# Kernel optimization log

Measured on AMD Instinct MI355X. Metric: run time of the kernel, lower is better.

The kernel has to match this reference:

```python
import jax, jax.numpy as jnp
import numpy as np

N_NODES = 100000
N_EDGES = 3200000
IN_FEATS, HID_FEATS, OUT_FEATS = 256, 128, 64


def setup_inputs() -> dict:
    key = jax.random.key(0)
    k1, k2, k3, k4, k5 = jax.random.split(key, 5)
    x = jax.random.normal(k1, (N_NODES, IN_FEATS), dtype=jnp.float32)
    edge_src = jax.random.randint(k2, (N_EDGES,), 0, N_NODES, dtype=jnp.int64)
    edge_dst = jax.random.randint(k3, (N_EDGES,), 0, N_NODES, dtype=jnp.int64)
    # weights initialized like nn.Parameter(th.randn(...))
    W1 = jax.random.normal(k4, (IN_FEATS, HID_FEATS), dtype=jnp.float32)
    W2 = jax.random.normal(k5, (HID_FEATS, OUT_FEATS), dtype=jnp.float32)
    return {"x": x, "edge_src": edge_src, "edge_dst": edge_dst, "W1": W1, "W2": W2}


def _spmm_sum(h, edge_src, edge_dst, n_nodes):
    # gspmmv with norm flags False: out[d] = sum_{(s,d) in E} h[s]
    msgs = h[edge_src]  # [E, F] gather
    return jax.ops.segment_sum(msgs, edge_dst, num_segments=n_nodes)


def reference(x, edge_src, edge_dst, W1, W2):
    n = x.shape[0]
    h = x @ W1                                  # [N, hid]
    h = _spmm_sum(h, edge_src, edge_dst, n)     # SpMM aggregation
    h = jax.nn.relu(h)
    h = h @ W2                                  # [N, out]
    h = _spmm_sum(h, edge_src, edge_dst, n)
    return h
```

## Files before the change

kernel.cpp:

```cpp
#include <hip/hip_runtime.h>
#include <hip/hip_bf16.h>

#define N_NODES   100000
#define IN_F      256
#define HID_F     128
#define OUT_F     64

#define SCAN_CHUNK 512
#define NSCAN_BLK ((N_NODES + SCAN_CHUNK - 1) / SCAN_CHUNK)

#define NGROUP    8
#define GRANGE    (N_NODES / NGROUP)
#define FILL_BLKS 2048

__device__ __forceinline__ ushort f2bf(float f) {
    uint u = __float_as_uint(f);
    u += 0x7fffu + ((u >> 16) & 1u);
    return (ushort)(u >> 16);
}
__device__ __forceinline__ float bf2f_lo(uint u) { return __uint_as_float(u << 16); }
__device__ __forceinline__ float bf2f_hi(uint u) { return __uint_as_float(u & 0xffff0000u); }

__global__ __launch_bounds__(256) void gemm1_kernel(const float* __restrict__ x,
                                                    const float* __restrict__ W1,
                                                    ushort* __restrict__ h1) {
    __shared__ float xs[32][IN_F];
    const int tid = threadIdx.x;
    const int block_row = blockIdx.x * 32;

    {
        const float4* xg = reinterpret_cast<const float4*>(x + (size_t)block_row * IN_F);
        float4* xsv = reinterpret_cast<float4*>(&xs[0][0]);
#pragma unroll
        for (int i = 0; i < 8; ++i) {
            int idx = tid + i * 256;
            xsv[idx] = xg[idx];
        }
    }
    __syncthreads();

    const int cg = tid & 31;
    const int rg = tid >> 5;

    float acc[4][4] = {};
#pragma unroll 4
    for (int k = 0; k < IN_F; ++k) {
        const float4 w = *reinterpret_cast<const float4*>(W1 + (size_t)k * HID_F + cg * 4);
#pragma unroll
        for (int r = 0; r < 4; ++r) {
            const float xv = xs[rg * 4 + r][k];
            acc[r][0] = fmaf(xv, w.x, acc[r][0]);
            acc[r][1] = fmaf(xv, w.y, acc[r][1]);
            acc[r][2] = fmaf(xv, w.z, acc[r][2]);
            acc[r][3] = fmaf(xv, w.w, acc[r][3]);
        }
    }

#pragma unroll
    for (int r = 0; r < 4; ++r) {
        uint2 o;
        o.x = ((uint)f2bf(acc[r][1]) << 16) | (uint)f2bf(acc[r][0]);
        o.y = ((uint)f2bf(acc[r][3]) << 16) | (uint)f2bf(acc[r][2]);
        *reinterpret_cast<uint2*>(h1 + (size_t)(block_row + rg * 4 + r) * HID_F + cg * 4) = o;
    }
}

__global__ __launch_bounds__(256) void gemm2_kernel(const ushort* __restrict__ agg1,
                                                    const float* __restrict__ W2,
                                                    ushort* __restrict__ h2) {
    __shared__ float as_[32][HID_F];
    const int tid = threadIdx.x;
    const int block_row = blockIdx.x * 32;

    {
        const uint* ag = reinterpret_cast<const uint*>(agg1 + (size_t)block_row * HID_F);
        float* asf = &as_[0][0];
#pragma unroll
        for (int i = 0; i < 8; ++i) {
            int idx = tid + i * 256;
            uint u = ag[idx];
            asf[2 * idx]     = fmaxf(bf2f_lo(u), 0.f);
            asf[2 * idx + 1] = fmaxf(bf2f_hi(u), 0.f);
        }
    }
    __syncthreads();

    const int cg = tid & 15;
    const int rg = tid >> 4;

    float acc[2][4] = {};
#pragma unroll 4
    for (int k = 0; k < HID_F; ++k) {
        const float4 w = *reinterpret_cast<const float4*>(W2 + (size_t)k * OUT_F + cg * 4);
#pragma unroll
        for (int r = 0; r < 2; ++r) {
            const float xv = as_[rg * 2 + r][k];
            acc[r][0] = fmaf(xv, w.x, acc[r][0]);
            acc[r][1] = fmaf(xv, w.y, acc[r][1]);
            acc[r][2] = fmaf(xv, w.z, acc[r][2]);
            acc[r][3] = fmaf(xv, w.w, acc[r][3]);
        }
    }

#pragma unroll
    for (int r = 0; r < 2; ++r) {
        uint2 o;
        o.x = ((uint)f2bf(acc[r][1]) << 16) | (uint)f2bf(acc[r][0]);
        o.y = ((uint)f2bf(acc[r][3]) << 16) | (uint)f2bf(acc[r][2]);
        *reinterpret_cast<uint2*>(h2 + (size_t)(block_row + rg * 2 + r) * OUT_F + cg * 4) = o;
    }
}

__global__ __launch_bounds__(256) void hist_kernel(const int* __restrict__ dst,
                                                   int* __restrict__ counts, int n_edges) {
    int i = blockIdx.x * blockDim.x + threadIdx.x;
    const int stride = gridDim.x * blockDim.x;
    for (; i < n_edges; i += stride) atomicAdd(&counts[dst[i]], 1);
}

__global__ __launch_bounds__(256) void scan_reduce(const int* __restrict__ counts,
                                                   int* __restrict__ partials, int n) {
    __shared__ int sm[256];
    const int base = blockIdx.x * SCAN_CHUNK;
    const int t = threadIdx.x;
    int v = 0;
    for (int i = t; i < SCAN_CHUNK; i += 256) {
        int idx = base + i;
        if (idx < n) v += counts[idx];
    }
    sm[t] = v;
    __syncthreads();
    for (int off = 128; off > 0; off >>= 1) {
        if (t < off) sm[t] += sm[t + off];
        __syncthreads();
    }
    if (t == 0) partials[blockIdx.x] = sm[0];
}

__global__ __launch_bounds__(256) void scan_partials(const int* __restrict__ partials,
                                                     int* __restrict__ blockoff, int n) {
    __shared__ int a[256], b[256];
    const int t = threadIdx.x;
    a[t] = (t < n) ? partials[t] : 0;
    __syncthreads();
    int* cur = a; int* nxt = b;
    for (int off = 1; off < 256; off <<= 1) {
        nxt[t] = cur[t] + (t >= off ? cur[t - off] : 0);
        __syncthreads();
        int* tmp = cur; cur = nxt; nxt = tmp;
    }
    if (t < n) blockoff[t] = (t > 0) ? cur[t - 1] : 0;
}

__global__ __launch_bounds__(256) void scan_final(const int* __restrict__ counts,
                                                  const int* __restrict__ blockoff,
                                                  int* __restrict__ row_ptr,
                                                  int* __restrict__ cursor,
                                                  int n, int n_edges) {
    __shared__ int a[SCAN_CHUNK], b[SCAN_CHUNK];
    const int base = blockIdx.x * SCAN_CHUNK;
    const int t = threadIdx.x;
    for (int i = t; i < SCAN_CHUNK; i += 256) {
        int idx = base + i;
        a[i] = (idx < n) ? counts[idx] : 0;
    }
    __syncthreads();
    int* cur = a; int* nxt = b;
    for (int off = 1; off < SCAN_CHUNK; off <<= 1) {
        for (int i = t; i < SCAN_CHUNK; i += 256)
            nxt[i] = cur[i] + (i >= off ? cur[i - off] : 0);
        __syncthreads();
        int* tmp = cur; cur = nxt; nxt = tmp;
    }
    const int boff = blockoff[blockIdx.x];
    for (int i = t; i < SCAN_CHUNK; i += 256) {
        int idx = base + i;
        if (idx < n) {
            int ex = boff + (i > 0 ? cur[i - 1] : 0);
            row_ptr[idx] = ex;
            cursor[idx]  = ex;
        }
    }
    if (blockIdx.x == 0 && t == 0) row_ptr[n] = n_edges;
}

__global__ __launch_bounds__(256) void fill_part_kernel(const int* __restrict__ src,
                                                        const int* __restrict__ dst,
                                                        int* __restrict__ cursor,
                                                        int* __restrict__ csr_src,
                                                        int n_edges) {
    const int g  = blockIdx.x & (NGROUP - 1);
    const int lb = blockIdx.x >> 3;
    const int lo = g * GRANGE;
    const int hi = lo + GRANGE;
    const int stride = (FILL_BLKS / NGROUP) * 256;
    for (int i = lb * 256 + threadIdx.x; i < n_edges; i += stride) {
        const int d = __builtin_nontemporal_load(dst + i);
        if (d >= lo && d < hi) {
            const int s = __builtin_nontemporal_load(src + i);
            const int pos = atomicAdd(&cursor[d], 1);
            csr_src[pos] = s;
        }
    }
}

__global__ __launch_bounds__(256) void spmm1_kernel(const ushort* __restrict__ h,
                                                    const int* __restrict__ row_ptr,
                                                    const int* __restrict__ csr_src,
                                                    ushort* __restrict__ outb,
                                                    int n_nodes) {
    const int wid = blockIdx.x * 4 + (threadIdx.x >> 6);
    const int lane = threadIdx.x & 63;
    if (wid >= n_nodes) return;
    const int half = lane >> 5;
    const int sub  = lane & 31;

    const int beg = __builtin_amdgcn_readfirstlane(row_ptr[wid]);
    const int end = __builtin_amdgcn_readfirstlane(row_ptr[wid + 1]);

    float a0 = 0.f, a1 = 0.f, a2 = 0.f, a3 = 0.f;
    int j = beg;
#pragma unroll 2
    for (; j + 3 < end; j += 4) {
        const int s0 = __builtin_amdgcn_readfirstlane(csr_src[j + 0]);
        const int s1 = __builtin_amdgcn_readfirstlane(csr_src[j + 1]);
        const int s2 = __builtin_amdgcn_readfirstlane(csr_src[j + 2]);
        const int s3 = __builtin_amdgcn_readfirstlane(csr_src[j + 3]);
        const int sa = half ? s1 : s0;
        const int sb = half ? s3 : s2;
        const uint2 u = *reinterpret_cast<const uint2*>(h + (size_t)sa * HID_F + sub * 4);
        const uint2 v = *reinterpret_cast<const uint2*>(h + (size_t)sb * HID_F + sub * 4);
        a0 += bf2f_lo(u.x) + bf2f_lo(v.x);
        a1 += bf2f_hi(u.x) + bf2f_hi(v.x);
        a2 += bf2f_lo(u.y) + bf2f_lo(v.y);
        a3 += bf2f_hi(u.y) + bf2f_hi(v.y);
    }
    if (j + 1 < end) {
        const int s0 = __builtin_amdgcn_readfirstlane(csr_src[j + 0]);
        const int s1 = __builtin_amdgcn_readfirstlane(csr_src[j + 1]);
        const int sa = half ? s1 : s0;
        const uint2 u = *reinterpret_cast<const uint2*>(h + (size_t)sa * HID_F + sub * 4);
        a0 += bf2f_lo(u.x); a1 += bf2f_hi(u.x);
        a2 += bf2f_lo(u.y); a3 += bf2f_hi(u.y);
        j += 2;
    }
    if (j < end && half == 0) {
        const int s = csr_src[j];
        const uint2 u = *reinterpret_cast<const uint2*>(h + (size_t)s * HID_F + sub * 4);
        a0 += bf2f_lo(u.x); a1 += bf2f_hi(u.x);
        a2 += bf2f_lo(u.y); a3 += bf2f_hi(u.y);
    }

    a0 += __shfl_xor(a0, 32);
    a1 += __shfl_xor(a1, 32);
    a2 += __shfl_xor(a2, 32);
    a3 += __shfl_xor(a3, 32);

    if (half == 0) {
        uint2 o;
        o.x = ((uint)f2bf(a1) << 16) | (uint)f2bf(a0);
        o.y = ((uint)f2bf(a3) << 16) | (uint)f2bf(a2);
        *reinterpret_cast<uint2*>(outb + (size_t)wid * HID_F + sub * 4) = o;
    }
}

__global__ __launch_bounds__(256) void spmm2_kernel(const ushort* __restrict__ h,
                                                    const int* __restrict__ row_ptr,
                                                    const int* __restrict__ csr_src,
                                                    float* __restrict__ out,
                                                    int n_nodes) {
    const int wid = blockIdx.x * 4 + (threadIdx.x >> 6);
    const int lane = threadIdx.x & 63;
    if (wid >= n_nodes) return;
    const int q   = lane >> 4;
    const int sub = lane & 15;

    const int beg = __builtin_amdgcn_readfirstlane(row_ptr[wid]);
    const int end = __builtin_amdgcn_readfirstlane(row_ptr[wid + 1]);

    float a0 = 0.f, a1 = 0.f, a2 = 0.f, a3 = 0.f;
    int j = beg;
#pragma unroll 2
    for (; j + 3 < end; j += 4) {
        const int s0 = __builtin_amdgcn_readfirstlane(csr_src[j + 0]);
        const int s1 = __builtin_amdgcn_readfirstlane(csr_src[j + 1]);
        const int s2 = __builtin_amdgcn_readfirstlane(csr_src[j + 2]);
        const int s3 = __builtin_amdgcn_readfirstlane(csr_src[j + 3]);
        const int sel01 = (q & 1) ? s1 : s0;
        const int sel23 = (q & 1) ? s3 : s2;
        const int sa    = (q & 2) ? sel23 : sel01;
        const uint2 u = *reinterpret_cast<const uint2*>(h + (size_t)sa * OUT_F + sub * 4);
        a0 += bf2f_lo(u.x); a1 += bf2f_hi(u.x);
        a2 += bf2f_lo(u.y); a3 += bf2f_hi(u.y);
    }
    {
        const int rem = end - j;
        if (q < rem) {
            const int s = csr_src[j + q];
            const uint2 u = *reinterpret_cast<const uint2*>(h + (size_t)s * OUT_F + sub * 4);
            a0 += bf2f_lo(u.x); a1 += bf2f_hi(u.x);
            a2 += bf2f_lo(u.y); a3 += bf2f_hi(u.y);
        }
    }

    a0 += __shfl_xor(a0, 16); a1 += __shfl_xor(a1, 16);
    a2 += __shfl_xor(a2, 16); a3 += __shfl_xor(a3, 16);
    a0 += __shfl_xor(a0, 32); a1 += __shfl_xor(a1, 32);
    a2 += __shfl_xor(a2, 32); a3 += __shfl_xor(a3, 32);

    if (q == 0) {
        float4 o = make_float4(a0, a1, a2, a3);
        *reinterpret_cast<float4*>(out + (size_t)wid * OUT_F + sub * 4) = o;
    }
}

extern "C" void kernel_launch(void* const* d_in, const int* in_sizes, int n_in,
                              void* d_out, int out_size, void* d_ws, size_t ws_size,
                              hipStream_t stream) {
    const float* x    = (const float*)d_in[0];
    const int*   esrc = (const int*)d_in[1];
    const int*   edst = (const int*)d_in[2];
    const float* W1   = (const float*)d_in[3];
    const float* W2   = (const float*)d_in[4];
    float* out = (float*)d_out;

    const int n_edges = in_sizes[1];

    const size_t h1b = (size_t)N_NODES * HID_F * sizeof(ushort);
    char* w = (char*)d_ws;
    ushort* h1   = (ushort*)w;
    ushort* agg1 = (ushort*)(w + h1b);
    ushort* h2   = h1;
    char* p = w + 2 * h1b;
    int* row_ptr  = (int*)p;  p += (((size_t)(N_NODES + 1) * 4 + 255) / 256) * 256;
    int* counts   = (int*)p;  p += (((size_t)N_NODES * 4 + 255) / 256) * 256;
    int* cursor   = (int*)p;  p += (((size_t)N_NODES * 4 + 255) / 256) * 256;
    int* blockoff = (int*)p;  p += 1024;
    int* partials = (int*)p;  p += 1024;
    int* csr_src  = (int*)p;

    hipMemsetAsync(counts, 0, (size_t)N_NODES * 4, stream);
    hist_kernel<<<2048, 256, 0, stream>>>(edst, counts, n_edges);
    scan_reduce<<<NSCAN_BLK, 256, 0, stream>>>(counts, partials, N_NODES);
    scan_partials<<<1, 256, 0, stream>>>(partials, blockoff, NSCAN_BLK);
    scan_final<<<NSCAN_BLK, 256, 0, stream>>>(counts, blockoff, row_ptr, cursor,
                                              N_NODES, n_edges);
    fill_part_kernel<<<FILL_BLKS, 256, 0, stream>>>(esrc, edst, cursor, csr_src, n_edges);

    gemm1_kernel<<<N_NODES / 32, 256, 0, stream>>>(x, W1, h1);
    spmm1_kernel<<<(N_NODES + 3) / 4, 256, 0, stream>>>(h1, row_ptr, csr_src,
                                                        agg1, N_NODES);
    gemm2_kernel<<<N_NODES / 32, 256, 0, stream>>>(agg1, W2, h2);
    spmm2_kernel<<<(N_NODES + 3) / 4, 256, 0, stream>>>(h2, row_ptr, csr_src,
                                                        out, N_NODES);
}
```

Measured before the change: 774.2 us.

## Use bf16 MFMA instructions for both dense GEMMs with pre-transposed weights

Replaces the FP32 scalar-FMA GEMM kernels with wavefront-level MFMA 16x16x32 bf16 kernels for both the input projection and the hidden projection. A small kernel first converts W1 and W2 to bf16 and transposes them so each lane can load contiguous 8-element B fragments. Inputs x are now rounded to bf16 before multiplication, which lowers precision, and the outputs are written as scattered 2-byte stores, which may coalesce poorly.

Result: faster. 691.2 us (-10.7%).

```diff
diff --git a/kernel.cpp b/kernel.cpp
--- a/kernel.cpp
+++ b/kernel.cpp
@@ -13,6 +13,9 @@
 #define GRANGE    (N_NODES / NGROUP)
 #define FILL_BLKS 2048
 
+typedef __attribute__((ext_vector_type(8))) short short8v;
+typedef __attribute__((ext_vector_type(4))) float f32x4;
+
 __device__ __forceinline__ ushort f2bf(float f) {
     uint u = __float_as_uint(f);
     u += 0x7fffu + ((u >> 16) & 1u);
@@ -21,94 +24,105 @@
 __device__ __forceinline__ float bf2f_lo(uint u) { return __uint_as_float(u << 16); }
 __device__ __forceinline__ float bf2f_hi(uint u) { return __uint_as_float(u & 0xffff0000u); }
 
-__global__ __launch_bounds__(256) void gemm1_kernel(const float* __restrict__ x,
-                                                    const float* __restrict__ W1,
-                                                    ushort* __restrict__ h1) {
-    __shared__ float xs[32][IN_F];
-    const int tid = threadIdx.x;
-    const int block_row = blockIdx.x * 32;
-
-    {
-        const float4* xg = reinterpret_cast<const float4*>(x + (size_t)block_row * IN_F);
-        float4* xsv = reinterpret_cast<float4*>(&xs[0][0]);
-#pragma unroll
-        for (int i = 0; i < 8; ++i) {
-            int idx = tid + i * 256;
-            xsv[idx] = xg[idx];
-        }
-    }
-    __syncthreads();
-
-    const int cg = tid & 31;
-    const int rg = tid >> 5;
-
-    float acc[4][4] = {};
-#pragma unroll 4
-    for (int k = 0; k < IN_F; ++k) {
-        const float4 w = *reinterpret_cast<const float4*>(W1 + (size_t)k * HID_F + cg * 4);
+__global__ __launch_bounds__(256) void wtrans_kernel(const float* __restrict__ W1,
+                                                     const float* __restrict__ W2,
+                                                     ushort* __restrict__ w1t,
+                                                     ushort* __restrict__ w2t) {
+    const int b = blockIdx.x;
+    if (b < 64) {
+        const int base = b * 512;
+        for (int e = base + threadIdx.x; e < base + 512; e += 256) {
+            int k = e >> 7, c = e & 127;
+            w1t[c * 256 + k] = f2bf(W1[e]);
+        }
+    } else {
+        const int base = (b - 64) * 512;
+        for (int e = base + threadIdx.x; e < base + 512; e += 256) {
+            int k = e >> 6, c = e & 63;
+            w2t[c * 128 + k] = f2bf(W2[e]);
+        }
+    }
+}
+
+__global__ __launch_bounds__(256) void gemm1_mfma(const float* __restrict__ x,
+                                                  const ushort* __restrict__ w1t,
+                                                  ushort* __restrict__ h1) {
+    const int wid  = threadIdx.x >> 6;
+    const int lane = threadIdx.x & 63;
+    const int l15  = lane & 15;
+    const int kgrp = lane >> 4;
+    const long base = (long)blockIdx.x * 64 + wid * 16;
+
+    long arow = base + l15;
+    if (arow > N_NODES - 1) arow = N_NODES - 1;
+    const float* ap = x + arow * IN_F + kgrp * 8;
+
+    f32x4 acc[8] = {};
+
+#pragma unroll
+    for (int ks = 0; ks < 8; ++ks) {
+        const float4 af0 = *reinterpret_cast<const float4*>(ap + ks * 32);
+        const float4 af1 = *reinterpret_cast<const float4*>(ap + ks * 32 + 4);
+        short8v a;
+        a[0] = (short)f2bf(af0.x); a[1] = (short)f2bf(af0.y);
+        a[2] = (short)f2bf(af0.z); a[3] = (short)f2bf(af0.w);
+        a[4] = (short)f2bf(af1.x); a[5] = (short)f2bf(af1.y);
+        a[6] = (short)f2bf(af1.z); a[7] = (short)f2bf(af1.w);
+#pragma unroll
+        for (int ct = 0; ct < 8; ++ct) {
+            const short8v bfr = *reinterpret_cast<const short8v*>(
+                w1t + (size_t)(ct * 16 + l15) * 256 + ks * 32 + kgrp * 8);
+            acc[ct] = __builtin_amdgcn_mfma_f32_16x16x32_bf16(a, bfr, acc[ct], 0, 0, 0);
+        }
+    }
+
+#pragma unroll
+    for (int ct = 0; ct < 8; ++ct)
 #pragma unroll
         for (int r = 0; r < 4; ++r) {
-            const float xv = xs[rg * 4 + r][k];
-            acc[r][0] = fmaf(xv, w.x, acc[r][0]);
-            acc[r][1] = fmaf(xv, w.y, acc[r][1]);
-            acc[r][2] = fmaf(xv, w.z, acc[r][2]);
-            acc[r][3] = fmaf(xv, w.w, acc[r][3]);
-        }
-    }
-
-#pragma unroll
-    for (int r = 0; r < 4; ++r) {
-        uint2 o;
-        o.x = ((uint)f2bf(acc[r][1]) << 16) | (uint)f2bf(acc[r][0]);
-        o.y = ((uint)f2bf(acc[r][3]) << 16) | (uint)f2bf(acc[r][2]);
-        *reinterpret_cast<uint2*>(h1 + (size_t)(block_row + rg * 4 + r) * HID_F + cg * 4) = o;
-    }
-}
-
-__global__ __launch_bounds__(256) void gemm2_kernel(const ushort* __restrict__ agg1,
-                                                    const float* __restrict__ W2,
-                                                    ushort* __restrict__ h2) {
-    __shared__ float as_[32][HID_F];
-    const int tid = threadIdx.x;
-    const int block_row = blockIdx.x * 32;
-
-    {
-        const uint* ag = reinterpret_cast<const uint*>(agg1 + (size_t)block_row * HID_F);
-        float* asf = &as_[0][0];
-#pragma unroll
-        for (int i = 0; i < 8; ++i) {
-            int idx = tid + i * 256;
-            uint u = ag[idx];
-            asf[2 * idx]     = fmaxf(bf2f_lo(u), 0.f);
-            asf[2 * idx + 1] = fmaxf(bf2f_hi(u), 0.f);
-        }
-    }
-    __syncthreads();
-
-    const int cg = tid & 15;
-    const int rg = tid >> 4;
-
-    float acc[2][4] = {};
-#pragma unroll 4
-    for (int k = 0; k < HID_F; ++k) {
-        const float4 w = *reinterpret_cast<const float4*>(W2 + (size_t)k * OUT_F + cg * 4);
-#pragma unroll
-        for (int r = 0; r < 2; ++r) {
-            const float xv = as_[rg * 2 + r][k];
-            acc[r][0] = fmaf(xv, w.x, acc[r][0]);
-            acc[r][1] = fmaf(xv, w.y, acc[r][1]);
-            acc[r][2] = fmaf(xv, w.z, acc[r][2]);
-            acc[r][3] = fmaf(xv, w.w, acc[r][3]);
-        }
-    }
-
-#pragma unroll
-    for (int r = 0; r < 2; ++r) {
-        uint2 o;
-        o.x = ((uint)f2bf(acc[r][1]) << 16) | (uint)f2bf(acc[r][0]);
-        o.y = ((uint)f2bf(acc[r][3]) << 16) | (uint)f2bf(acc[r][2]);
-        *reinterpret_cast<uint2*>(h2 + (size_t)(block_row + rg * 2 + r) * OUT_F + cg * 4) = o;
-    }
+            const long orow = base + kgrp * 4 + r;
+            if (orow < N_NODES)
+                h1[orow * HID_F + ct * 16 + l15] = f2bf(acc[ct][r]);
+        }
+}
+
+__global__ __launch_bounds__(256) void gemm2_mfma(const ushort* __restrict__ agg1,
+                                                  const ushort* __restrict__ w2t,
+                                                  ushort* __restrict__ h2) {
+    const int wid  = threadIdx.x >> 6;
+    const int lane = threadIdx.x & 63;
+    const int l15  = lane & 15;
+    const int kgrp = lane >> 4;
+    const long base = (long)blockIdx.x * 64 + wid * 16;
+
+    long arow = base + l15;
+    if (arow > N_NODES - 1) arow = N_NODES - 1;
+    const ushort* ap = agg1 + arow * HID_F + kgrp * 8;
+
+    f32x4 acc[4] = {};
+
+#pragma unroll
+    for (int ks = 0; ks < 4; ++ks) {
+        short8v a = *reinterpret_cast<const short8v*>(ap + ks * 32);
+#pragma unroll
+        for (int i = 0; i < 8; ++i)
+            if (a[i] < 0) a[i] = 0;
+#pragma unroll
+        for (int ct = 0; ct < 4; ++ct) {
+            const short8v bfr = *reinterpret_cast<const short8v*>(
+                w2t + (size_t)(ct * 16 + l15) * 128 + ks * 32 + kgrp * 8);
+            acc[ct] = __builtin_amdgcn_mfma_f32_16x16x32_bf16(a, bfr, acc[ct], 0, 0, 0);
+        }
+    }
+
+#pragma unroll
+    for (int ct = 0; ct < 4; ++ct)
+#pragma unroll
+        for (int r = 0; r < 4; ++r) {
+            const long orow = base + kgrp * 4 + r;
+            if (orow < N_NODES)
+                h2[orow * OUT_F + ct * 16 + l15] = f2bf(acc[ct][r]);
+        }
 }
 
 __global__ __launch_bounds__(256) void hist_kernel(const int* __restrict__ dst,
@@ -337,8 +351,11 @@
     int* cursor   = (int*)p;  p += (((size_t)N_NODES * 4 + 255) / 256) * 256;
     int* blockoff = (int*)p;  p += 1024;
     int* partials = (int*)p;  p += 1024;
-    int* csr_src  = (int*)p;
-
+    int* csr_src  = (int*)p;  p += (size_t)n_edges * 4;
+    ushort* w1t   = (ushort*)p;  p += 128 * 256 * 2;
+    ushort* w2t   = (ushort*)p;
+
+    wtrans_kernel<<<80, 256, 0, stream>>>(W1, W2, w1t, w2t);
     hipMemsetAsync(counts, 0, (size_t)N_NODES * 4, stream);
     hist_kernel<<<2048, 256, 0, stream>>>(edst, counts, n_edges);
     scan_reduce<<<NSCAN_BLK, 256, 0, stream>>>(counts, partials, N_NODES);
@@ -347,10 +364,12 @@
                                               N_NODES, n_edges);
     fill_part_kernel<<<FILL_BLKS, 256, 0, stream>>>(esrc, edst, cursor, csr_src, n_edges);
 
-    gemm1_kernel<<<N_NODES / 32, 256, 0, stream>>>(x, W1, h1);
+    const int gemm_blocks = (N_NODES + 63) / 64;
+
+    gemm1_mfma<<<gemm_blocks, 256, 0, stream>>>(x, w1t, h1);
     spmm1_kernel<<<(N_NODES + 3) / 4, 256, 0, stream>>>(h1, row_ptr, csr_src,
                                                         agg1, N_NODES);
-    gemm2_kernel<<<N_NODES / 32, 256, 0, stream>>>(agg1, W2, h2);
+    gemm2_mfma<<<gemm_blocks, 256, 0, stream>>>(agg1, w2t, h2);
     spmm2_kernel<<<(N_NODES + 3) / 4, 256, 0, stream>>>(h2, row_ptr, csr_src,
                                                         out, N_NODES);
 }
```
